# Kernel tuning notes

Hardware: AMD Instinct MI355X
Metric: run time of the kernel (lower is better)

The kernel has to match this reference:

```python
import jax, jax.numpy as jnp
import numpy as np

D = 256          # feature_dim
H = 4            # num_heads (hard-coded in AdaAttentionalPropagation)
HD = D // H      # per-head dim = 64
L = 6            # number of layers
B, N, M = 2, 2048, 2048
NAMES = ("self", "cross", "self", "cross", "self", "cross")
POOLS = (1, 1, 2, 2, 2, 2)
EPS = 1e-5


def conv1x1(W, b, x):
    # Conv1d kernel_size=1 == pointwise linear over channels: x [B, Cin, N] -> [B, Cout, N]
    return jnp.einsum('oi,bin->bon', W, x) + b[None, :, None]


def inst_norm(x):
    # InstanceNorm1d(affine=False): normalize over spatial dim per (batch, channel)
    mu = jnp.mean(x, axis=-1, keepdims=True)
    var = jnp.var(x, axis=-1, keepdims=True)
    return (x - mu) * jax.lax.rsqrt(var + EPS)


def attn_prop(params, x, source, mask):
    # One AdaAttentionalPropagation layer. x [B,D,Nq], source [B,D,Nk], mask [B,Nq,Nk]
    Wq, bq, Wk, bk, Wv, bv, Wm, bm, W1, b1, W2, b2 = params
    b = x.shape[0]
    q = conv1x1(Wq, bq, x).reshape(b, HD, H, -1)       # [B, hd, H, Nq]
    k = conv1x1(Wk, bk, source).reshape(b, HD, H, -1)  # [B, hd, H, Nk]
    v = conv1x1(Wv, bv, source).reshape(b, HD, H, -1)
    scores = jnp.einsum('bdhn,bdhm->bhnm', q, k) / np.sqrt(HD).astype(np.float32)
    scores = scores * mask[:, None]                     # multiplicative pruned mask
    prob = jax.nn.softmax(scores, axis=-1)              # [B, H, Nq, Nk]
    att = jnp.einsum('bhnm,bdhm->bdhn', prob, v).reshape(b, D, -1)
    message = conv1x1(Wm, bm, att)                      # merge
    y = jnp.concatenate([x, message], axis=1)           # [B, 2D, Nq]
    h = jax.nn.relu(inst_norm(conv1x1(W1, b1, y)))      # MLP_IN hidden
    delta = conv1x1(W2, b2, h)                          # [B, D, Nq]
    return delta, jnp.mean(prob, axis=1)                # prob averaged over heads


def prune(conn, prob, pool, k_cur):
    # update_connections_by_pooling_size: keep top (k_cur // pool) entries per row
    if prob is None or pool == 1:
        return conn, k_cur
    k_new = k_cur // pool
    vals, idxs = jax.lax.top_k(prob, k_new)             # over last axis
    b, n, _ = conn.shape
    new = jnp.zeros_like(conn).at[
        jnp.arange(b)[:, None, None], jnp.arange(n)[None, :, None], idxs
    ].set(jnp.where(vals > 0, 1.0, 0.0).astype(conn.dtype))
    return jax.lax.stop_gradient(new), k_new


def setup_inputs() -> dict:
    key = jax.random.key(0)
    ks = jax.random.split(key, 16)
    s1 = 1.0 / np.sqrt(D)
    s2 = 1.0 / np.sqrt(2 * D)
    return {
        "desc0": jax.random.normal(ks[0], (B, D, N), dtype=jnp.float32),
        "desc1": jax.random.normal(ks[1], (B, D, M), dtype=jnp.float32),
        "Wq": jax.random.normal(ks[2], (L, D, D), dtype=jnp.float32) * s1,
        "bq": jax.random.normal(ks[3], (L, D), dtype=jnp.float32) * 0.01,
        "Wk": jax.random.normal(ks[4], (L, D, D), dtype=jnp.float32) * s1,
        "bk": jax.random.normal(ks[5], (L, D), dtype=jnp.float32) * 0.01,
        "Wv": jax.random.normal(ks[6], (L, D, D), dtype=jnp.float32) * s1,
        "bv": jax.random.normal(ks[7], (L, D), dtype=jnp.float32) * 0.01,
        "Wm": jax.random.normal(ks[8], (L, D, D), dtype=jnp.float32) * s1,
        "bm": jax.random.normal(ks[9], (L, D), dtype=jnp.float32) * 0.01,
        "W1": jax.random.normal(ks[10], (L, 2 * D, 2 * D), dtype=jnp.float32) * s2,
        "b1": jax.random.normal(ks[11], (L, 2 * D), dtype=jnp.float32) * 0.01,
        "W2": jax.random.normal(ks[12], (L, D, 2 * D), dtype=jnp.float32) * s2,
        "b2": jnp.zeros((L, D), dtype=jnp.float32),  # nn.init.constant_(mlp[-1].bias, 0)
    }


def reference(desc0, desc1, Wq, bq, Wk, bk, Wv, bv, Wm, bm, W1, b1, W2, b2):
    b = desc0.shape[0]
    n, m = desc0.shape[2], desc1.shape[2]
    masks = {
        '00': jnp.ones((b, n, n), jnp.float32), '01': jnp.ones((b, n, m), jnp.float32),
        '11': jnp.ones((b, m, m), jnp.float32), '10': jnp.ones((b, m, n), jnp.float32),
    }
    probs = {'00': None, '01': None, '11': None, '10': None}
    kcnt = {'00': n, '01': m, '11': m, '10': n}
    for i in range(L):
        params = (Wq[i], bq[i], Wk[i], bk[i], Wv[i], bv[i],
                  Wm[i], bm[i], W1[i], b1[i], W2[i], b2[i])
        pool = POOLS[i]
        if NAMES[i] == 'cross':
            masks['01'], kcnt['01'] = prune(masks['01'], probs['01'], pool, kcnt['01'])
            delta0, probs['01'] = attn_prop(params, desc0, desc1, masks['01'])
            masks['10'], kcnt['10'] = prune(masks['10'], probs['10'], pool, kcnt['10'])
            delta1, probs['10'] = attn_prop(params, desc1, desc0, masks['10'])
        else:
            masks['00'], kcnt['00'] = prune(masks['00'], probs['00'], pool, kcnt['00'])
            delta0, probs['00'] = attn_prop(params, desc0, desc0, masks['00'])
            masks['11'], kcnt['11'] = prune(masks['11'], probs['11'], pool, kcnt['11'])
            delta1, probs['11'] = attn_prop(params, desc1, desc1, masks['11'])
        desc0 = desc0 + delta0
        desc1 = desc1 + delta1
    return jnp.stack([desc0, desc1])  # [2, B, D, N]
```

## Files before the change

kernel.cpp:

```cpp
#include <hip/hip_runtime.h>
#include <hip/hip_bf16.h>
#include <stdint.h>

#define NPTS 2048
#define MB_ROW 256L
#define MB_B   ((long)NPTS * MB_ROW)
#define MB_T   (2 * MB_B)

typedef __attribute__((ext_vector_type(8))) short bf16x8;
typedef __attribute__((ext_vector_type(4))) float f32x4;
#define MFMA16 __builtin_amdgcn_mfma_f32_16x16x32_bf16

__device__ inline unsigned short f2b(float f) {
  union { float f; unsigned int u; } x; x.f = f;
  unsigned int u = x.u;
  return (unsigned short)((u + 0x7FFFu + ((u >> 16) & 1u)) >> 16);
}
__device__ inline float bfu(unsigned int us) {
  union { unsigned int u; float f; } x; x.u = (us & 0xFFFFu) << 16;
  return x.f;
}
__device__ inline void sp3(float x, unsigned short& h, unsigned short& m, unsigned short& l) {
  h = f2b(x);
  float r1 = x - bfu(h);
  m = f2b(r1);
  l = f2b(r1 - bfu(m));
}
__device__ inline void gld16(const unsigned short* g, unsigned short* l) {
  __builtin_amdgcn_global_load_lds(
      (const __attribute__((address_space(1))) void*)g,
      (__attribute__((address_space(3))) void*)l, 16, 0, 0);
}
__device__ inline int swzF(int F) { return F ^ ((F >> 3) & 7); }

#define E_P3  0
#define E_V3  1
#define E_S3  2
#define E_Y3  3
#define E_H   4
#define E_RES 5
#define E_S3S 6

template <int EPI>
__global__ __launch_bounds__(256) void t3_k(
    const unsigned short* __restrict__ A, long aps,
    const unsigned short* __restrict__ B, long bps,
    const unsigned short* __restrict__ B2, long b2ps,
    const float* __restrict__ bias,
    void* __restrict__ out,
    const unsigned char* __restrict__ masks,
    int K, int lda, int ldb, int ksplit, long sps,
    int zbase, int xorv, int selfl, int yoff) {
  const int t = threadIdx.x;
  const int z = blockIdx.z;
  const int zg = zbase + z;
  long aoff = 0, boff = 0, b2off = 0;
  if constexpr (EPI == E_P3 || EPI == E_V3) {
    boff = (long)z * 524288;
  } else if constexpr (EPI == E_S3 || EPI == E_S3S) {
    const int sb = zg >> 2, h = zg & 3;
    aoff = (long)zg * 131072;
    boff = (long)((sb ^ xorv) * 4 + h) * 131072;
  } else if constexpr (EPI == E_Y3) {
    boff = (long)zg * 524288;
  } else if constexpr (EPI == E_H) {
    boff = (long)zg * 524288;
    b2off = (long)z * 524288;
  } else {
    boff = (long)z * 1048576;
  }
  const int n0 = blockIdx.x * 64;
  const int m0 = ((EPI == E_S3 || EPI == E_S3S) ? yoff : 0) + blockIdx.y * 64;

  __shared__ __align__(16) unsigned short As[3][64 * 64];
  __shared__ __align__(16) unsigned short Bs[3][64 * 64];
  __shared__ unsigned int Ms[128];
  if constexpr (EPI == E_S3 || EPI == E_S3S) {
    if (t < 128) {
      const int sb = zg >> 2;
      const int type = selfl ? (sb >> 1) : 2 + (sb >> 1);
      const unsigned int* mw =
          (const unsigned int*)(masks + (long)type * MB_T + (long)(sb & 1) * MB_B);
      Ms[t] = mw[(long)(m0 + (t >> 1)) * 64 + (n0 >> 5) + (t & 1)];
    }
  }

  const int w = t >> 6;
  const int L = t & 63;
  const int wm = (w & 1) * 32, wn = (w >> 1) * 32;
  const int lr = t & 15, lk = (t >> 4) & 3;
  const int swr = (lr & 7) << 3;
  const int grow = (L >> 3);
  const int gj = L & 7;

  f32x4 acc[2][2];
#pragma unroll
  for (int i = 0; i < 2; ++i)
#pragma unroll
    for (int j = 0; j < 2; ++j) acc[i][j] = (f32x4){0.f, 0.f, 0.f, 0.f};

  for (int k0 = 0; k0 < K; k0 += 64) {
    const unsigned short* Bsel;
    long bo, bp;
    int kb;
    if (k0 < ksplit) { Bsel = B; bo = boff; bp = bps; kb = k0; }
    else             { Bsel = B2; bo = b2off; bp = b2ps; kb = k0 - ksplit; }
    if (k0) __syncthreads();
#pragma unroll
    for (int pl = 0; pl < 3; ++pl) {
      const unsigned short* Ap = A + (long)pl * aps + aoff;
      const unsigned short* Bp = Bsel + (long)pl * bp + bo;
#pragma unroll
      for (int c = 0; c < 2; ++c) {
        const int rbase = w * 16 + c * 8;
        const int row = rbase + grow;
        const int colA = (gj ^ (row & 7)) << 3;
        gld16(&Ap[(long)(m0 + row) * lda + k0 + colA], &As[pl][rbase * 64]);
        gld16(&Bp[(long)(n0 + row) * ldb + kb + colA], &Bs[pl][rbase * 64]);
      }
    }
    __syncthreads();
#pragma unroll
    for (int kk = 0; kk < 2; ++kk) {
      bf16x8 af[3][2], bf[3][2];
#pragma unroll
      for (int pl = 0; pl < 3; ++pl)
#pragma unroll
        for (int mi = 0; mi < 2; ++mi) {
          af[pl][mi] = *(const bf16x8*)&As[pl][(wm + mi * 16 + lr) * 64 + ((kk * 32 + lk * 8) ^ swr)];
          bf[pl][mi] = *(const bf16x8*)&Bs[pl][(wn + mi * 16 + lr) * 64 + ((kk * 32 + lk * 8) ^ swr)];
        }
#pragma unroll
      for (int mi = 0; mi < 2; ++mi)
#pragma unroll
        for (int ni = 0; ni < 2; ++ni) {
          f32x4 c = acc[mi][ni];
          c = MFMA16(af[2][mi], bf[0][ni], c, 0, 0, 0);
          c = MFMA16(af[0][mi], bf[2][ni], c, 0, 0, 0);
          c = MFMA16(af[1][mi], bf[1][ni], c, 0, 0, 0);
          c = MFMA16(af[1][mi], bf[0][ni], c, 0, 0, 0);
          c = MFMA16(af[0][mi], bf[1][ni], c, 0, 0, 0);
          c = MFMA16(af[0][mi], bf[0][ni], c, 0, 0, 0);
          acc[mi][ni] = c;
        }
    }
  }

  if constexpr (EPI == E_S3 || EPI == E_S3S) {
    __syncthreads();
    float* ST = (float*)&As[0][0];
#pragma unroll
    for (int mi = 0; mi < 2; ++mi)
#pragma unroll
      for (int ni = 0; ni < 2; ++ni)
#pragma unroll
        for (int r = 0; r < 4; ++r)
          ST[(wm + mi * 16 + lk * 4 + r) * 68 + wn + ni * 16 + lr] = acc[mi][ni][r];
    __syncthreads();
    float* o = (float*)out;
#pragma unroll
    for (int it = 0; it < 4; ++it) {
      const int row = (t >> 4) + it * 16;
      const int col = (t & 15) * 4;
      float4 vv = *(const float4*)&ST[row * 68 + col];
      const unsigned int mw = Ms[row * 2 + (col >> 5)];
      vv.x = ((mw >> ((col + 0) & 31)) & 1u) ? vv.x * 0.125f : 0.f;
      vv.y = ((mw >> ((col + 1) & 31)) & 1u) ? vv.y * 0.125f : 0.f;
      vv.z = ((mw >> ((col + 2) & 31)) & 1u) ? vv.z * 0.125f : 0.f;
      vv.w = ((mw >> ((col + 3) & 31)) & 1u) ? vv.w * 0.125f : 0.f;
      const int rloc = blockIdx.y * 64 + row;
      *(float4*)&o[(long)z * sps + (long)rloc * 2048 + n0 + col] = vv;
      if constexpr (EPI == E_S3S) {
        float2* pst = (float2*)const_cast<float*>(bias);
        const int CHrows = (int)(sps >> 11);
        float mx4 = fmaxf(fmaxf(vv.x, vv.y), fmaxf(vv.z, vv.w));
#pragma unroll
        for (int oo = 1; oo < 16; oo <<= 1) mx4 = fmaxf(mx4, __shfl_xor(mx4, oo));
        float e4 = __expf(vv.x - mx4) + __expf(vv.y - mx4) +
                   __expf(vv.z - mx4) + __expf(vv.w - mx4);
#pragma unroll
        for (int oo = 1; oo < 16; oo <<= 1) e4 += __shfl_xor(e4, oo);
        if ((t & 15) == 0)
          pst[((long)z * CHrows + rloc) * 32 + blockIdx.x] = make_float2(mx4, e4);
      }
    }
    return;
  }

#pragma unroll
  for (int mi = 0; mi < 2; ++mi) {
#pragma unroll
    for (int ni = 0; ni < 2; ++ni) {
      f32x4 a = acc[mi][ni];
      const int cM = m0 + wm + mi * 16 + lk * 4;
      const int pN = n0 + wn + ni * 16 + lr;
      if constexpr (EPI == E_P3) {
        float4 bv4 = *(const float4*)&bias[cM];
        float bb[4] = {bv4.x, bv4.y, bv4.z, bv4.w};
        unsigned short* o = (unsigned short*)out;
        const long b0 = (long)z * 524288 + (long)pN * 64 + (cM >> 2);
#pragma unroll
        for (int r = 0; r < 4; ++r) {
          unsigned short h_, m_, l_;
          sp3(a[r] + bb[r], h_, m_, l_);
          const long ad = b0 + (long)r * 131072;
          o[ad] = h_; o[ad + 2097152] = m_; o[ad + 4194304] = l_;
        }
      } else if constexpr (EPI == E_V3) {
        float4 bv4 = *(const float4*)&bias[cM];
        float bb[4] = {bv4.x, bv4.y, bv4.z, bv4.w};
        unsigned short* o = (unsigned short*)out;
        const long b0 = (long)z * 524288 + (long)(cM >> 2) * 2048 + pN;
#pragma unroll
        for (int r = 0; r < 4; ++r) {
          unsigned short h_, m_, l_;
          sp3(a[r] + bb[r], h_, m_, l_);
          const long ad = b0 + (long)r * 131072;
          o[ad] = h_; o[ad + 2097152] = m_; o[ad + 4194304] = l_;
        }
      } else if constexpr (EPI == E_Y3) {
        float4 bv4 = *(const float4*)&bias[cM];
        float bb[4] = {bv4.x, bv4.y, bv4.z, bv4.w};
        unsigned short* o = (unsigned short*)out;
        ushort4 h4, m4, l4;
        unsigned short* hp = (unsigned short*)&h4;
        unsigned short* mp = (unsigned short*)&m4;
        unsigned short* lp = (unsigned short*)&l4;
#pragma unroll
        for (int r = 0; r < 4; ++r) sp3(a[r] + bb[r], hp[r], mp[r], lp[r]);
        const long b0 = (long)z * 524288 + (long)pN * 256 + cM;
        *(ushort4*)&o[b0] = h4;
        *(ushort4*)&o[b0 + sps] = m4;
        *(ushort4*)&o[b0 + 2 * sps] = l4;
      } else if constexpr (EPI == E_H) {
        *(f32x4*)&((float*)out)[(long)z * 1048576 + (long)pN * 512 + cM] = a;
      } else {
        float4 bv4 = *(const float4*)&bias[cM];
        float* p = &((float*)out)[(long)zg * 524288 + (long)pN * 256 + cM];
        float4 old = *(const float4*)p;
        float4 nw;
        nw.x = old.x + a[0] + bv4.x; nw.y = old.y + a[1] + bv4.y;
        nw.z = old.z + a[2] + bv4.z; nw.w = old.w + a[3] + bv4.w;
        *(float4*)p = nw;
      }
    }
  }
}

__global__ __launch_bounds__(256) void stat_k(const float2* __restrict__ pst,
                                              float2* __restrict__ stats) {
  const int idx = blockIdx.x * 256 + threadIdx.x;
  const float2* p = pst + (long)idx * 32;
  float m = p[0].x;
#pragma unroll
  for (int i = 1; i < 32; ++i) m = fmaxf(m, p[i].x);
  float s = 0.f;
#pragma unroll
  for (int i = 0; i < 32; ++i) s += p[i].y * __expf(p[i].x - m);
  stats[idx] = make_float2(m, 1.0f / s);
}

__global__ __launch_bounds__(256) void softmax_prune_k(
    const float* __restrict__ S, float2* __restrict__ stats,
    unsigned char* __restrict__ masks,
    int knew, int sbG, int cb, int selfl, long sps, int CH) {
  const int t = threadIdx.x;
  const int lane = t & 63;
  const int wv = t >> 6;
  const int nl = blockIdx.x;

  __shared__ __align__(16) float4 pL4[4][512];
  __shared__ int hist[256];
  __shared__ int wred[4];
  __shared__ int sbx[2];

  {
    const float* row = S + (long)wv * sps + (long)nl * 2048 + lane * 32;
    float xs[32];
#pragma unroll
    for (int e = 0; e < 8; ++e) {
      float4 u = *(const float4*)(row + e * 4);
      xs[e * 4 + 0] = u.x; xs[e * 4 + 1] = u.y;
      xs[e * 4 + 2] = u.z; xs[e * 4 + 3] = u.w;
    }
    float m = xs[0];
#pragma unroll
    for (int j = 1; j < 32; ++j) m = fmaxf(m, xs[j]);
    for (int o = 32; o; o >>= 1) m = fmaxf(m, __shfl_xor(m, o));
    float s = 0.f;
#pragma unroll
    for (int j = 0; j < 32; ++j) { xs[j] = __expf(xs[j] - m); s += xs[j]; }
    for (int o = 32; o; o >>= 1) s += __shfl_xor(s, o);
    const float ri = 1.0f / s;
    if (lane == 0) stats[(long)wv * CH + nl] = make_float2(m, ri);
#pragma unroll
    for (int e = 0; e < 8; ++e) {
      float4 pv;
      pv.x = xs[e * 4 + 0] * ri; pv.y = xs[e * 4 + 1] * ri;
      pv.z = xs[e * 4 + 2] * ri; pv.w = xs[e * 4 + 3] * ri;
      pL4[wv][swzF(lane * 8 + e)] = pv;
    }
  }
  __syncthreads();

  unsigned int key[8];
  {
#pragma unroll
    for (int jj = 0; jj < 2; ++jj) {
      const int Fs = swzF(t * 2 + jj);
      float4 p0 = pL4[0][Fs];
      float4 p1 = pL4[1][Fs];
      float4 p2 = pL4[2][Fs];
      float4 p3 = pL4[3][Fs];
      float4 mm;
      mm.x = 0.25f * p0.x; mm.x += 0.25f * p1.x; mm.x += 0.25f * p2.x; mm.x += 0.25f * p3.x;
      mm.y = 0.25f * p0.y; mm.y += 0.25f * p1.y; mm.y += 0.25f * p2.y; mm.y += 0.25f * p3.y;
      mm.z = 0.25f * p0.z; mm.z += 0.25f * p1.z; mm.z += 0.25f * p2.z; mm.z += 0.25f * p3.z;
      mm.w = 0.25f * p0.w; mm.w += 0.25f * p1.w; mm.w += 0.25f * p2.w; mm.w += 0.25f * p3.w;
      key[jj * 4 + 0] = __float_as_uint(mm.x);
      key[jj * 4 + 1] = __float_as_uint(mm.y);
      key[jj * 4 + 2] = __float_as_uint(mm.z);
      key[jj * 4 + 3] = __float_as_uint(mm.w);
    }
  }

  unsigned int pref = 0;
  int kneed = knew;
  for (int pass = 0; pass < 4; ++pass) {
    const int shift = 24 - pass * 8;
    hist[t] = 0;
    __syncthreads();
    const unsigned int hm = (pass == 0) ? 0u : (0xFFFFFFFFu << (shift + 8));
#pragma unroll
    for (int j = 0; j < 8; ++j) {
      unsigned int k = key[j];
      if ((k & hm) == pref) atomicAdd(&hist[(k >> shift) & 255], 1);
    }
    __syncthreads();
    const int h = hist[t];
    int s = h;
#pragma unroll
    for (int o = 1; o < 64; o <<= 1) {
      int tmp = __shfl_down(s, o);
      if (lane + o < 64) s += tmp;
    }
    if (lane == 0) wred[wv] = s;
    __syncthreads();
    int addhi = 0;
#pragma unroll
    for (int w2 = 0; w2 < 4; ++w2)
      if (w2 > wv) addhi += wred[w2];
    s += addhi;
    const int above = s - h;
    if (s >= kneed && above < kneed) { sbx[0] = t; sbx[1] = above; }
    __syncthreads();
    pref |= ((unsigned int)sbx[0]) << shift;
    kneed -= sbx[1];
    __syncthreads();
  }
  const unsigned int T = pref;
  const int take = kneed;
  int cnt = 0;
#pragma unroll
  for (int j = 0; j < 8; ++j) cnt += (key[j] == T);
  int pc = cnt;
#pragma unroll
  for (int o = 1; o < 64; o <<= 1) {
    int tmp = __shfl_up(pc, o);
    if (lane >= o) pc += tmp;
  }
  if (lane == 63) wred[wv] = pc;
  __syncthreads();
  int woff = 0;
#pragma unroll
  for (int w2 = 0; w2 < 4; ++w2)
    if (w2 < wv) woff += wred[w2];
  int base = woff + pc - cnt;
  unsigned int byte = 0;
#pragma unroll
  for (int j = 0; j < 8; ++j) {
    unsigned int k = key[j];
    int sel = 0;
    if (k > T) sel = 1;
    else if (k == T) { if (T > 0u && base < take) sel = 1; base++; }
    byte |= (unsigned int)sel << j;
  }
  const int type = selfl ? (sbG >> 1) : 2 + (sbG >> 1);
  unsigned char* mb = masks + (long)type * MB_T + (long)(sbG & 1) * MB_B;
  mb[(long)(cb + nl) * MB_ROW + t] = (unsigned char)byte;
}

__global__ __launch_bounds__(256) void pv3_k(
    const unsigned short* __restrict__ V3, const float* __restrict__ S, long sps,
    const float2* __restrict__ stats, int CH,
    float* __restrict__ part, int zbase, int xorv) {
  const int t = threadIdx.x;
  const int h = blockIdx.z;
  const int kseg = blockIdx.y;
  const int n0 = blockIdx.x * 64;
  const int sb = zbase >> 2;
  const unsigned short* Vb = V3 + (long)((sb ^ xorv) * 4 + h) * 131072;
  const float* Sp = S + (long)h * sps;
  const float2* sth = stats + (long)h * CH;

  __shared__ __align__(16) unsigned short Bs[3][64 * 64];

  const int w = t >> 6;
  const int wm = (w & 1) * 32, wn = (w >> 1) * 32;
  const int lr = t & 15, lk = (t >> 4) & 3;
  const int srow = t >> 3, scol = (t & 7) * 8;
  const int sws = scol ^ ((srow & 7) << 3);
  const int swr = (lr & 7) << 3;

  f32x4 acc[2][2];
#pragma unroll
  for (int i = 0; i < 2; ++i)
#pragma unroll
    for (int j = 0; j < 2; ++j) acc[i][j] = (f32x4){0.f, 0.f, 0.f, 0.f};

  const int kbeg = kseg * 256;
  const float2 st0 = sth[n0 + srow];
  const float2 st1 = sth[n0 + 32 + srow];
  const float* srcA = &Sp[(long)(n0 + srow) * 2048 + kbeg + scol];
  const float* srcB = &Sp[(long)(n0 + 32 + srow) * 2048 + kbeg + scol];

  float4 c0a = *(const float4*)srcA;
  float4 c0b = *(const float4*)(srcA + 4);
  float4 c1a = *(const float4*)srcB;
  float4 c1b = *(const float4*)(srcB + 4);

#pragma unroll
  for (int ki = 0; ki < 4; ++ki) {
    const int k0 = kbeg + ki * 64;
    float4 n0a, n0b, n1a, n1b;
    if (ki < 3) {
      const int off = (ki + 1) * 64;
      n0a = *(const float4*)(srcA + off);
      n0b = *(const float4*)(srcA + off + 4);
      n1a = *(const float4*)(srcB + off);
      n1b = *(const float4*)(srcB + off + 4);
    }
    if (ki) __syncthreads();
    {
      float xs[8] = {c0a.x, c0a.y, c0a.z, c0a.w, c0b.x, c0b.y, c0b.z, c0b.w};
      ushort4 hq[2], mq[2], lq[2];
      unsigned short* hp = (unsigned short*)hq;
      unsigned short* mp = (unsigned short*)mq;
      unsigned short* lp = (unsigned short*)lq;
#pragma unroll
      for (int j = 0; j < 8; ++j) {
        float p = __expf(xs[j] - st0.x) * st0.y;
        sp3(p, hp[j], mp[j], lp[j]);
      }
      *(ushort4*)&Bs[0][srow * 64 + sws] = hq[0];
      *(ushort4*)&Bs[0][srow * 64 + sws + 4] = hq[1];
      *(ushort4*)&Bs[1][srow * 64 + sws] = mq[0];
      *(ushort4*)&Bs[1][srow * 64 + sws + 4] = mq[1];
      *(ushort4*)&Bs[2][srow * 64 + sws] = lq[0];
      *(ushort4*)&Bs[2][srow * 64 + sws + 4] = lq[1];
    }
    {
      float xs[8] = {c1a.x, c1a.y, c1a.z, c1a.w, c1b.x, c1b.y, c1b.z, c1b.w};
      ushort4 hq[2], mq[2], lq[2];
      unsigned short* hp = (unsigned short*)hq;
      unsigned short* mp = (unsigned short*)mq;
      unsigned short* lp = (unsigned short*)lq;
#pragma unroll
      for (int j = 0; j < 8; ++j) {
        float p = __expf(xs[j] - st1.x) * st1.y;
        sp3(p, hp[j], mp[j], lp[j]);
      }
      const int rr = 32 + srow;
      *(ushort4*)&Bs[0][rr * 64 + sws] = hq[0];
      *(ushort4*)&Bs[0][rr * 64 + sws + 4] = hq[1];
      *(ushort4*)&Bs[1][rr * 64 + sws] = mq[0];
      *(ushort4*)&Bs[1][rr * 64 + sws + 4] = mq[1];
      *(ushort4*)&Bs[2][rr * 64 + sws] = lq[0];
      *(ushort4*)&Bs[2][rr * 64 + sws + 4] = lq[1];
    }
    __syncthreads();
#pragma unroll
    for (int kk = 0; kk < 2; ++kk) {
      bf16x8 af[3][2], bf[3][2];
#pragma unroll
      for (int pl = 0; pl < 3; ++pl) {
#pragma unroll
        for (int mi = 0; mi < 2; ++mi) {
          af[pl][mi] = *(const bf16x8*)&Vb[(long)pl * 2097152 +
                                           (long)(wm + mi * 16 + lr) * 2048 + k0 + kk * 32 + lk * 8];
          bf[pl][mi] = *(const bf16x8*)&Bs[pl][(wn + mi * 16 + lr) * 64 + ((kk * 32 + lk * 8) ^ swr)];
        }
      }
#pragma unroll
      for (int mi = 0; mi < 2; ++mi)
#pragma unroll
        for (int ni = 0; ni < 2; ++ni) {
          f32x4 c = acc[mi][ni];
          c = MFMA16(af[2][mi], bf[0][ni], c, 0, 0, 0);
          c = MFMA16(af[0][mi], bf[2][ni], c, 0, 0, 0);
          c = MFMA16(af[1][mi], bf[1][ni], c, 0, 0, 0);
          c = MFMA16(af[1][mi], bf[0][ni], c, 0, 0, 0);
          c = MFMA16(af[0][mi], bf[1][ni], c, 0, 0, 0);
          c = MFMA16(af[0][mi], bf[0][ni], c, 0, 0, 0);
          acc[mi][ni] = c;
        }
    }
    if (ki < 3) { c0a = n0a; c0b = n0b; c1a = n1a; c1b = n1b; }
  }

  float* pp = part + (((long)kseg * 4 + h) * CH) * 64;
#pragma unroll
  for (int mi = 0; mi < 2; ++mi) {
#pragma unroll
    for (int ni = 0; ni < 2; ++ni) {
      const int cM = wm + mi * 16 + lk * 4;
      const int pN = n0 + wn + ni * 16 + lr;
      *(f32x4*)&pp[(long)pN * 64 + cM] = acc[mi][ni];
    }
  }
}

__global__ __launch_bounds__(256) void comb_k(const float* __restrict__ part,
                                              unsigned short* __restrict__ att3,
                                              int CH, int sb, int cb) {
  const int q = threadIdx.x & 63;
  const int g = threadIdx.x >> 6;
  const int nl = blockIdx.x * 4 + g;
  float s[4] = {0.f, 0.f, 0.f, 0.f};
#pragma unroll
  for (int ks = 0; ks < 8; ++ks)
#pragma unroll
    for (int h = 0; h < 4; ++h)
      s[h] += part[(((long)ks * 4 + h) * CH + nl) * 64 + q];
  ushort4 h4, m4, l4;
  unsigned short* hp = (unsigned short*)&h4;
  unsigned short* mp = (unsigned short*)&m4;
  unsigned short* lp = (unsigned short*)&l4;
#pragma unroll
  for (int h = 0; h < 4; ++h) sp3(s[h], hp[h], mp[h], lp[h]);
  const long base = (long)sb * 524288 + (long)(cb + nl) * 256 + 4 * q;
  *(ushort4*)&att3[base] = h4;
  *(ushort4*)&att3[base + 2097152] = m4;
  *(ushort4*)&att3[base + 4194304] = l4;
}

__global__ __launch_bounds__(256) void inormA_k(const float* __restrict__ H,
                                                float* __restrict__ partial) {
  const int seg = blockIdx.x, sbl = blockIdx.y;
  const float* hp = H + (long)sbl * 1048576;
  const int t = threadIdx.x;
  float s0 = 0.f, q0 = 0.f, s1 = 0.f, q1 = 0.f;
  const int r0 = seg * 64;
  for (int r = r0; r < r0 + 64; ++r) {
    float x0 = hp[(long)r * 512 + t];
    float x1 = hp[(long)r * 512 + t + 256];
    s0 += x0; q0 = fmaf(x0, x0, q0);
    s1 += x1; q1 = fmaf(x1, x1, q1);
  }
  float* pp = partial + ((long)sbl * 32 + seg) * 1024;
  pp[t] = s0; pp[t + 256] = s1;
  pp[512 + t] = q0; pp[512 + t + 256] = q1;
}

__global__ __launch_bounds__(256) void inormB_k(const float* __restrict__ partial,
                                                float* __restrict__ stats2) {
  const int sbl = blockIdx.x;
  const int t = threadIdx.x;
  const float* pp = partial + (long)sbl * 32768;
  float a0 = 0.f, b0 = 0.f, a1 = 0.f, b1 = 0.f;
  for (int seg = 0; seg < 32; ++seg) {
    const float* p = pp + seg * 1024;
    a0 += p[t]; a1 += p[t + 256];
    b0 += p[512 + t]; b1 += p[512 + t + 256];
  }
  float mu0 = a0 * (1.f / 2048.f);
  float mu1 = a1 * (1.f / 2048.f);
  float rs0 = rsqrtf(b0 * (1.f / 2048.f) - mu0 * mu0 + 1e-5f);
  float rs1 = rsqrtf(b1 * (1.f / 2048.f) - mu1 * mu1 + 1e-5f);
  float* st = stats2 + (long)sbl * 1024;
  st[t] = mu0; st[t + 256] = mu1;
  st[512 + t] = rs0; st[512 + t + 256] = rs1;
}

__global__ __launch_bounds__(256) void inormC_k(const float* __restrict__ H,
                                                const float* __restrict__ stats2,
                                                unsigned short* __restrict__ HB,
                                                long hps) {
  const int seg = blockIdx.x, sbl = blockIdx.y;
  const float* hp = H + (long)sbl * 1048576;
  unsigned short* hb = HB + (long)sbl * 1048576;
  const float* st = stats2 + (long)sbl * 1024;
  const int t = threadIdx.x;
  const float mu0 = st[t], mu1 = st[t + 256];
  const float rs0 = st[512 + t], rs1 = st[512 + t + 256];
  const int r0 = seg * 64;
  for (int r = r0; r < r0 + 64; ++r) {
    float x0 = hp[(long)r * 512 + t];
    float x1 = hp[(long)r * 512 + t + 256];
    float o0 = (x0 - mu0) * rs0; o0 = o0 > 0.f ? o0 : 0.f;
    float o1 = (x1 - mu1) * rs1; o1 = o1 > 0.f ? o1 : 0.f;
    unsigned short h_, m_, l_;
    sp3(o0, h_, m_, l_);
    const long ad0 = (long)r * 512 + t;
    hb[ad0] = h_; hb[ad0 + hps] = m_; hb[ad0 + 2 * hps] = l_;
    sp3(o1, h_, m_, l_);
    const long ad1 = ad0 + 256;
    hb[ad1] = h_; hb[ad1 + hps] = m_; hb[ad1 + 2 * hps] = l_;
  }
}

__global__ __launch_bounds__(256) void split6_k(
    const float* __restrict__ q, const float* __restrict__ k,
    const float* __restrict__ v, const float* __restrict__ m,
    const float* __restrict__ w1, const float* __restrict__ w2,
    unsigned short* __restrict__ dst) {
  long i = ((long)blockIdx.x * 256 + threadIdx.x) * 4;
  const float* src;
  long off, base, ps;
  if (i < 262144) {
    int sel = (int)(i >> 16);
    src = sel == 0 ? q : sel == 1 ? k : sel == 2 ? v : m;
    off = i & 65535; base = (long)sel * 196608; ps = 65536;
  } else if (i < 524288) {
    src = w1; off = i - 262144; base = 786432; ps = 262144;
  } else {
    src = w2; off = i - 524288; base = 1572864; ps = 131072;
  }
  float4 vv = *(const float4*)&src[off];
  float xs[4] = {vv.x, vv.y, vv.z, vv.w};
  ushort4 h4, m4, l4;
  unsigned short* hp = (unsigned short*)&h4;
  unsigned short* mp = (unsigned short*)&m4;
  unsigned short* lp = (unsigned short*)&l4;
#pragma unroll
  for (int j = 0; j < 4; ++j) sp3(xs[j], hp[j], mp[j], lp[j]);
  *(ushort4*)&dst[base + off] = h4;
  *(ushort4*)&dst[base + ps + off] = m4;
  *(ushort4*)&dst[base + 2 * ps + off] = l4;
}

__global__ __launch_bounds__(256) void split3_k(const float* __restrict__ src,
                                                unsigned short* __restrict__ dst,
                                                long plane, long n) {
  long i = ((long)blockIdx.x * 256 + threadIdx.x) * 4;
  if (i >= n) return;
  float4 v = *(const float4*)&src[i];
  float xs[4] = {v.x, v.y, v.z, v.w};
  ushort4 h4, m4, l4;
  unsigned short* hp = (unsigned short*)&h4;
  unsigned short* mp = (unsigned short*)&m4;
  unsigned short* lp = (unsigned short*)&l4;
#pragma unroll
  for (int j = 0; j < 4; ++j) sp3(xs[j], hp[j], mp[j], lp[j]);
  *(ushort4*)&dst[i] = h4;
  *(ushort4*)&dst[plane + i] = m4;
  *(ushort4*)&dst[2 * plane + i] = l4;
}

__global__ __launch_bounds__(256) void tin_k(const float* __restrict__ d0,
                                             const float* __restrict__ d1,
                                             float* __restrict__ descT) {
  __shared__ float tl[32][33];
  const int sb = blockIdx.z, s = sb >> 1, b = sb & 1;
  const float* src = (s ? d1 : d0) + (long)b * 524288;
  const int p0 = blockIdx.x * 32, c0 = blockIdx.y * 32;
  const int tx = threadIdx.x & 31, ty = threadIdx.x >> 5;
#pragma unroll
  for (int i = 0; i < 4; ++i)
    tl[ty + i * 8][tx] = src[(long)(c0 + ty + i * 8) * 2048 + p0 + tx];
  __syncthreads();
#pragma unroll
  for (int i = 0; i < 4; ++i)
    descT[(long)sb * 524288 + (long)(p0 + ty + i * 8) * 256 + c0 + tx] = tl[tx][ty + i * 8];
}

__global__ __launch_bounds__(256) void tout_k(const float* __restrict__ descT,
                                              float* __restrict__ out) {
  __shared__ float tl[32][33];
  const int sb = blockIdx.z;
  const int p0 = blockIdx.x * 32, c0 = blockIdx.y * 32;
  const int tx = threadIdx.x & 31, ty = threadIdx.x >> 5;
#pragma unroll
  for (int i = 0; i < 4; ++i)
    tl[ty + i * 8][tx] = descT[(long)sb * 524288 + (long)(p0 + ty + i * 8) * 256 + c0 + tx];
  __syncthreads();
#pragma unroll
  for (int i = 0; i < 4; ++i)
    out[(long)sb * 524288 + (long)(c0 + ty + i * 8) * 2048 + p0 + tx] = tl[tx][ty + i * 8];
}

extern "C" void kernel_launch(void* const* d_in, const int* in_sizes, int n_in,
                              void* d_out, int out_size, void* d_ws, size_t ws_size,
                              hipStream_t stream) {
  (void)in_sizes; (void)n_in; (void)out_size;
  const float* in_d0 = (const float*)d_in[0];
  const float* in_d1 = (const float*)d_in[1];
  const float* Wq = (const float*)d_in[2];
  const float* bq = (const float*)d_in[3];
  const float* Wk = (const float*)d_in[4];
  const float* bk = (const float*)d_in[5];
  const float* Wv = (const float*)d_in[6];
  const float* bv = (const float*)d_in[7];
  const float* Wm = (const float*)d_in[8];
  const float* bm = (const float*)d_in[9];
  const float* W1 = (const float*)d_in[10];
  const float* b1 = (const float*)d_in[11];
  const float* W2 = (const float*)d_in[12];
  const float* b2 = (const float*)d_in[13];
  (void)b1;

  const long region_b = (long)ws_size - 79429632;
  const int CH = (region_b >= 40992L * 2048) ? 2048
               : (region_b >= 40992L * 1024) ? 1024 : 512;
  const int nchunks = 2048 / CH;
  const long sps = (long)CH * 2048;
  const int mb = (region_b >= 4 * 13766656L) ? 4 : (region_b >= 2 * 13766656L) ? 2 : 1;

  uint8_t* w = (uint8_t*)d_ws;
  float* descT          = (float*)w;
  unsigned short* desc3 = (unsigned short*)(w + 8388608);
  unsigned short* Q3    = (unsigned short*)(w + 20971520);
  unsigned short* K3    = (unsigned short*)(w + 33554432);
  unsigned short* V3    = (unsigned short*)(w + 46137344);
  unsigned short* att3  = (unsigned short*)(w + 58720256);
  unsigned short* wbuf  = (unsigned short*)(w + 71303168);
  unsigned char* masks  = w + 75235328;
  uint8_t* region       = w + 79429632;
  float* S              = (float*)region;
  float* part           = (float*)(region + (long)CH * 32768);
  float2* pst           = (float2*)part;
  float2* stats         = (float2*)(region + (long)CH * 32768 + (long)CH * 8192);
  unsigned short* msg3  = (unsigned short*)region;
  float* hbuf           = (float*)(region + (long)mb * 3145728);
  unsigned short* hB3   = (unsigned short*)(region + (long)mb * 7340032);
  float* inpart         = (float*)(region + (long)mb * 13631488);
  float* instats        = (float*)(region + (long)mb * 13631488 + (long)mb * 131072);

  const unsigned short* wq3 = wbuf;
  const unsigned short* wk3 = wbuf + 196608;
  const unsigned short* wv3 = wbuf + 393216;
  const unsigned short* wm3 = wbuf + 589824;
  const unsigned short* w13 = wbuf + 786432;
  const unsigned short* w23 = wbuf + 1572864;

  tin_k<<<dim3(64, 8, 4), 256, 0, stream>>>(in_d0, in_d1, descT);
  hipMemsetAsync(masks, 0xFF, 4 * MB_T, stream);

  for (int l = 0; l < 6; ++l) {
    const int selfl = (l % 2 == 0);
    const int xorv = selfl ? 0 : 2;
    const int knew = (l < 2) ? 1024 : (l < 4) ? 512 : 0;

    split6_k<<<dim3(640), 256, 0, stream>>>(Wq + (long)l * 65536, Wk + (long)l * 65536,
                                            Wv + (long)l * 65536, Wm + (long)l * 65536,
                                            W1 + (long)l * 262144, W2 + (long)l * 131072,
                                            wbuf);
    split3_k<<<dim3(2048), 256, 0, stream>>>(descT, desc3, 2097152, 2097152);

    t3_k<E_P3><<<dim3(32, 4, 4), 256, 0, stream>>>(
        wq3, 65536, desc3, 2097152, nullptr, 0, bq + l * 256, Q3, nullptr,
        256, 256, 256, 1 << 30, 0, 0, 0, 0, 0);
    t3_k<E_P3><<<dim3(32, 4, 4), 256, 0, stream>>>(
        wk3, 65536, desc3, 2097152, nullptr, 0, bk + l * 256, K3, nullptr,
        256, 256, 256, 1 << 30, 0, 0, 0, 0, 0);
    t3_k<E_V3><<<dim3(32, 4, 4), 256, 0, stream>>>(
        wv3, 65536, desc3, 2097152, nullptr, 0, bv + l * 256, V3, nullptr,
        256, 256, 256, 1 << 30, 0, 0, 0, 0, 0);

    for (int sb = 0; sb < 4; ++sb) {
      for (int c = 0; c < nchunks; ++c) {
        const int cb = c * CH;
        if (knew) {
          t3_k<E_S3><<<dim3(32, CH / 64, 4), 256, 0, stream>>>(
              Q3, 2097152, K3, 2097152, nullptr, 0, nullptr, S, masks,
              64, 64, 64, 1 << 30, sps, sb * 4, xorv, selfl, cb);
          softmax_prune_k<<<dim3(CH), 256, 0, stream>>>(
              S, stats, masks, knew, sb, cb, selfl, sps, CH);
        } else {
          t3_k<E_S3S><<<dim3(32, CH / 64, 4), 256, 0, stream>>>(
              Q3, 2097152, K3, 2097152, nullptr, 0, (const float*)pst, S, masks,
              64, 64, 64, 1 << 30, sps, sb * 4, xorv, selfl, cb);
          stat_k<<<dim3(4 * CH / 256), 256, 0, stream>>>(pst, stats);
        }
        pv3_k<<<dim3(CH / 64, 8, 4), 256, 0, stream>>>(V3, S, sps, stats, CH, part, sb * 4, xorv);
        comb_k<<<dim3(CH / 4), 256, 0, stream>>>(part, att3, CH, sb, cb);
      }
    }

    for (int p = 0; p < 4; p += mb) {
      t3_k<E_Y3><<<dim3(32, 4, mb), 256, 0, stream>>>(
          wm3, 65536, att3, 2097152, nullptr, 0, bm + l * 256, msg3, nullptr,
          256, 256, 256, 1 << 30, (long)mb * 524288, p, 0, 0, 0);
      t3_k<E_H><<<dim3(32, 8, mb), 256, 0, stream>>>(
          w13, 262144, desc3, 2097152, msg3, (long)mb * 524288, nullptr, hbuf, nullptr,
          512, 512, 256, 256, 0, p, 0, 0, 0);
      inormA_k<<<dim3(32, mb), 256, 0, stream>>>(hbuf, inpart);
      inormB_k<<<dim3(mb), 256, 0, stream>>>(inpart, instats);
      inormC_k<<<dim3(32, mb), 256, 0, stream>>>(hbuf, instats, hB3, (long)mb * 1048576);
      t3_k<E_RES><<<dim3(32, 4, mb), 256, 0, stream>>>(
          w23, 131072, hB3, (long)mb * 1048576, nullptr, 0, b2 + l * 256, descT, nullptr,
          512, 512, 512, 1 << 30, 0, p, 0, 0, 0);
    }
  }

  tout_k<<<dim3(64, 8, 4), 256, 0, stream>>>(descT, (float*)d_out);
}
```

Before: 2.834 ms.

## Split QK^T score GEMM into dedicated kernel with 64x128 tiles

Moves the attention score (QK^T) GEMM out of the generic t3_k template into a dedicated s3w_k kernel. Each block now computes a 64x128 tile instead of 64x64, and the whole K=64 slab of all three bf16 split planes is loaded into LDS once, with no k-loop. The wider tile lets each Q fragment be reused across four N sub-tiles and halves the grid. In exchange it uses more LDS and registers per block, which may lower occupancy. The mask, scale and partial-softmax-stats epilogue is widened to 8 columns per thread, writing two stat entries per 128-wide tile so the stat_k layout stays the same.

```diff
diff --git a/kernel.cpp b/kernel.cpp
--- a/kernel.cpp
+++ b/kernel.cpp
@@ -35,11 +35,9 @@
 
 #define E_P3  0
 #define E_V3  1
-#define E_S3  2
 #define E_Y3  3
 #define E_H   4
 #define E_RES 5
-#define E_S3S 6
 
 template <int EPI>
 __global__ __launch_bounds__(256) void t3_k(
@@ -57,10 +55,6 @@
   long aoff = 0, boff = 0, b2off = 0;
   if constexpr (EPI == E_P3 || EPI == E_V3) {
     boff = (long)z * 524288;
-  } else if constexpr (EPI == E_S3 || EPI == E_S3S) {
-    const int sb = zg >> 2, h = zg & 3;
-    aoff = (long)zg * 131072;
-    boff = (long)((sb ^ xorv) * 4 + h) * 131072;
   } else if constexpr (EPI == E_Y3) {
     boff = (long)zg * 524288;
   } else if constexpr (EPI == E_H) {
@@ -70,20 +64,10 @@
     boff = (long)z * 1048576;
   }
   const int n0 = blockIdx.x * 64;
-  const int m0 = ((EPI == E_S3 || EPI == E_S3S) ? yoff : 0) + blockIdx.y * 64;
+  const int m0 = blockIdx.y * 64;
 
   __shared__ __align__(16) unsigned short As[3][64 * 64];
   __shared__ __align__(16) unsigned short Bs[3][64 * 64];
-  __shared__ unsigned int Ms[128];
-  if constexpr (EPI == E_S3 || EPI == E_S3S) {
-    if (t < 128) {
-      const int sb = zg >> 2;
-      const int type = selfl ? (sb >> 1) : 2 + (sb >> 1);
-      const unsigned int* mw =
-          (const unsigned int*)(masks + (long)type * MB_T + (long)(sb & 1) * MB_B);
-      Ms[t] = mw[(long)(m0 + (t >> 1)) * 64 + (n0 >> 5) + (t & 1)];
-    }
-  }
 
   const int w = t >> 6;
   const int L = t & 63;
@@ -144,47 +128,6 @@
           acc[mi][ni] = c;
         }
     }
-  }
-
-  if constexpr (EPI == E_S3 || EPI == E_S3S) {
-    __syncthreads();
-    float* ST = (float*)&As[0][0];
-#pragma unroll
-    for (int mi = 0; mi < 2; ++mi)
-#pragma unroll
-      for (int ni = 0; ni < 2; ++ni)
-#pragma unroll
-        for (int r = 0; r < 4; ++r)
-          ST[(wm + mi * 16 + lk * 4 + r) * 68 + wn + ni * 16 + lr] = acc[mi][ni][r];
-    __syncthreads();
-    float* o = (float*)out;
-#pragma unroll
-    for (int it = 0; it < 4; ++it) {
-      const int row = (t >> 4) + it * 16;
-      const int col = (t & 15) * 4;
-      float4 vv = *(const float4*)&ST[row * 68 + col];
-      const unsigned int mw = Ms[row * 2 + (col >> 5)];
-      vv.x = ((mw >> ((col + 0) & 31)) & 1u) ? vv.x * 0.125f : 0.f;
-      vv.y = ((mw >> ((col + 1) & 31)) & 1u) ? vv.y * 0.125f : 0.f;
-      vv.z = ((mw >> ((col + 2) & 31)) & 1u) ? vv.z * 0.125f : 0.f;
-      vv.w = ((mw >> ((col + 3) & 31)) & 1u) ? vv.w * 0.125f : 0.f;
-      const int rloc = blockIdx.y * 64 + row;
-      *(float4*)&o[(long)z * sps + (long)rloc * 2048 + n0 + col] = vv;
-      if constexpr (EPI == E_S3S) {
-        float2* pst = (float2*)const_cast<float*>(bias);
-        const int CHrows = (int)(sps >> 11);
-        float mx4 = fmaxf(fmaxf(vv.x, vv.y), fmaxf(vv.z, vv.w));
-#pragma unroll
-        for (int oo = 1; oo < 16; oo <<= 1) mx4 = fmaxf(mx4, __shfl_xor(mx4, oo));
-        float e4 = __expf(vv.x - mx4) + __expf(vv.y - mx4) +
-                   __expf(vv.z - mx4) + __expf(vv.w - mx4);
-#pragma unroll
-        for (int oo = 1; oo < 16; oo <<= 1) e4 += __shfl_xor(e4, oo);
-        if ((t & 15) == 0)
-          pst[((long)z * CHrows + rloc) * 32 + blockIdx.x] = make_float2(mx4, e4);
-      }
-    }
-    return;
   }
 
 #pragma unroll
@@ -243,6 +186,145 @@
         nw.z = old.z + a[2] + bv4.z; nw.w = old.w + a[3] + bv4.w;
         *(float4*)p = nw;
       }
+    }
+  }
+}
+
+template <int STATS>
+__global__ __launch_bounds__(256) void s3w_k(
+    const unsigned short* __restrict__ Q3, const unsigned short* __restrict__ K3,
+    float* __restrict__ S, float2* __restrict__ pst,
+    const unsigned char* __restrict__ masks,
+    long sps, int zbase, int xorv, int selfl, int yoff) {
+  const int t = threadIdx.x;
+  const int z = blockIdx.z;
+  const int zg = zbase + z;
+  const int sb = zg >> 2, h = zg & 3;
+  const long aoff = (long)zg * 131072;
+  const long boff = (long)((sb ^ xorv) * 4 + h) * 131072;
+  const int n0 = blockIdx.x * 128;
+  const int m0 = yoff + blockIdx.y * 64;
+
+  __shared__ __align__(16) unsigned short sh[3 * 4096 + 3 * 8192];
+  unsigned short* Asp = sh;
+  unsigned short* Bsp = sh + 12288;
+  __shared__ unsigned int Ms[256];
+  {
+    const int type = selfl ? (sb >> 1) : 2 + (sb >> 1);
+    const unsigned int* mw =
+        (const unsigned int*)(masks + (long)type * MB_T + (long)(sb & 1) * MB_B);
+    Ms[t] = mw[(long)(m0 + (t >> 2)) * 64 + (n0 >> 5) + (t & 3)];
+  }
+
+  const int w = t >> 6;
+  const int L = t & 63;
+  const int lr = t & 15, lk = (t >> 4) & 3;
+  const int swr = (lr & 7) << 3;
+  const int grow = L >> 3;
+  const int gj = L & 7;
+  const int wm = (w & 1) * 32, wn = (w >> 1) * 64;
+
+#pragma unroll
+  for (int pl = 0; pl < 3; ++pl) {
+    const unsigned short* Ap = Q3 + (long)pl * 2097152 + aoff;
+    const unsigned short* Bp = K3 + (long)pl * 2097152 + boff;
+#pragma unroll
+    for (int c = 0; c < 2; ++c) {
+      const int rbase = w * 16 + c * 8;
+      const int row = rbase + grow;
+      const int colA = (gj ^ (row & 7)) << 3;
+      gld16(&Ap[(long)(m0 + row) * 64 + colA], &Asp[pl * 4096 + rbase * 64]);
+    }
+#pragma unroll
+    for (int c = 0; c < 4; ++c) {
+      const int rbase = w * 32 + c * 8;
+      const int row = rbase + grow;
+      const int colA = (gj ^ (row & 7)) << 3;
+      gld16(&Bp[(long)(n0 + row) * 64 + colA], &Bsp[pl * 8192 + rbase * 64]);
+    }
+  }
+  __syncthreads();
+
+  f32x4 acc[2][4];
+#pragma unroll
+  for (int i = 0; i < 2; ++i)
+#pragma unroll
+    for (int j = 0; j < 4; ++j) acc[i][j] = (f32x4){0.f, 0.f, 0.f, 0.f};
+
+#pragma unroll
+  for (int kk = 0; kk < 2; ++kk) {
+    bf16x8 af[3][2];
+#pragma unroll
+    for (int pl = 0; pl < 3; ++pl)
+#pragma unroll
+      for (int mi = 0; mi < 2; ++mi)
+        af[pl][mi] = *(const bf16x8*)&Asp[pl * 4096 + (wm + mi * 16 + lr) * 64 + ((kk * 32 + lk * 8) ^ swr)];
+#pragma unroll
+    for (int ni = 0; ni < 4; ++ni) {
+      bf16x8 bfx[3];
+#pragma unroll
+      for (int pl = 0; pl < 3; ++pl)
+        bfx[pl] = *(const bf16x8*)&Bsp[pl * 8192 + (wn + ni * 16 + lr) * 64 + ((kk * 32 + lk * 8) ^ swr)];
+#pragma unroll
+      for (int mi = 0; mi < 2; ++mi) {
+        f32x4 c = acc[mi][ni];
+        c = MFMA16(af[2][mi], bfx[0], c, 0, 0, 0);
+        c = MFMA16(af[0][mi], bfx[2], c, 0, 0, 0);
+        c = MFMA16(af[1][mi], bfx[1], c, 0, 0, 0);
+        c = MFMA16(af[1][mi], bfx[0], c, 0, 0, 0);
+        c = MFMA16(af[0][mi], bfx[1], c, 0, 0, 0);
+        c = MFMA16(af[0][mi], bfx[0], c, 0, 0, 0);
+        acc[mi][ni] = c;
+      }
+    }
+  }
+
+  __syncthreads();
+  float* ST = (float*)sh;
+#pragma unroll
+  for (int mi = 0; mi < 2; ++mi)
+#pragma unroll
+    for (int ni = 0; ni < 4; ++ni)
+#pragma unroll
+      for (int r = 0; r < 4; ++r)
+        ST[(wm + mi * 16 + lk * 4 + r) * 132 + wn + ni * 16 + lr] = acc[mi][ni][r];
+  __syncthreads();
+  float* o = S;
+  const int CHrows = (int)(sps >> 11);
+#pragma unroll
+  for (int it = 0; it < 4; ++it) {
+    const int row = (t >> 4) + it * 16;
+    const int col = (t & 15) * 8;
+    float4 v0 = *(const float4*)&ST[row * 132 + col];
+    float4 v1 = *(const float4*)&ST[row * 132 + col + 4];
+    const unsigned int mw = Ms[row * 4 + (col >> 5)];
+    v0.x = ((mw >> ((col + 0) & 31)) & 1u) ? v0.x * 0.125f : 0.f;
+    v0.y = ((mw >> ((col + 1) & 31)) & 1u) ? v0.y * 0.125f : 0.f;
+    v0.z = ((mw >> ((col + 2) & 31)) & 1u) ? v0.z * 0.125f : 0.f;
+    v0.w = ((mw >> ((col + 3) & 31)) & 1u) ? v0.w * 0.125f : 0.f;
+    v1.x = ((mw >> ((col + 4) & 31)) & 1u) ? v1.x * 0.125f : 0.f;
+    v1.y = ((mw >> ((col + 5) & 31)) & 1u) ? v1.y * 0.125f : 0.f;
+    v1.z = ((mw >> ((col + 6) & 31)) & 1u) ? v1.z * 0.125f : 0.f;
+    v1.w = ((mw >> ((col + 7) & 31)) & 1u) ? v1.w * 0.125f : 0.f;
+    const int rloc = blockIdx.y * 64 + row;
+    *(float4*)&o[(long)z * sps + (long)rloc * 2048 + n0 + col] = v0;
+    *(float4*)&o[(long)z * sps + (long)rloc * 2048 + n0 + col + 4] = v1;
+    if constexpr (STATS) {
+      float mx8 = fmaxf(fmaxf(fmaxf(v0.x, v0.y), fmaxf(v0.z, v0.w)),
+                        fmaxf(fmaxf(v1.x, v1.y), fmaxf(v1.z, v1.w)));
+      mx8 = fmaxf(mx8, __shfl_xor(mx8, 1));
+      mx8 = fmaxf(mx8, __shfl_xor(mx8, 2));
+      mx8 = fmaxf(mx8, __shfl_xor(mx8, 4));
+      float e8 = __expf(v0.x - mx8) + __expf(v0.y - mx8) +
+                 __expf(v0.z - mx8) + __expf(v0.w - mx8) +
+                 __expf(v1.x - mx8) + __expf(v1.y - mx8) +
+                 __expf(v1.z - mx8) + __expf(v1.w - mx8);
+      e8 += __shfl_xor(e8, 1);
+      e8 += __shfl_xor(e8, 2);
+      e8 += __shfl_xor(e8, 4);
+      if ((t & 7) == 0)
+        pst[((long)z * CHrows + rloc) * 32 + blockIdx.x * 2 + ((t >> 3) & 1)] =
+            make_float2(mx8, e8);
     }
   }
 }
@@ -771,15 +853,13 @@
       for (int c = 0; c < nchunks; ++c) {
         const int cb = c * CH;
         if (knew) {
-          t3_k<E_S3><<<dim3(32, CH / 64, 4), 256, 0, stream>>>(
-              Q3, 2097152, K3, 2097152, nullptr, 0, nullptr, S, masks,
-              64, 64, 64, 1 << 30, sps, sb * 4, xorv, selfl, cb);
+          s3w_k<0><<<dim3(16, CH / 64, 4), 256, 0, stream>>>(
+              Q3, K3, S, pst, masks, sps, sb * 4, xorv, selfl, cb);
           softmax_prune_k<<<dim3(CH), 256, 0, stream>>>(
               S, stats, masks, knew, sb, cb, selfl, sps, CH);
         } else {
-          t3_k<E_S3S><<<dim3(32, CH / 64, 4), 256, 0, stream>>>(
-              Q3, 2097152, K3, 2097152, nullptr, 0, (const float*)pst, S, masks,
-              64, 64, 64, 1 << 30, sps, sb * 4, xorv, selfl, cb);
+          s3w_k<1><<<dim3(16, CH / 64, 4), 256, 0, stream>>>(
+              Q3, K3, S, pst, masks, sps, sb * 4, xorv, selfl, cb);
           stat_k<<<dim3(4 * CH / 256), 256, 0, stream>>>(pst, stats);
         }
         pv3_k<<<dim3(CH / 64, 8, 4), 256, 0, stream>>>(V3, S, sps, stats, CH, part, sb * 4, xorv);
```

Measured after the change: 2.906 ms. 2.6% more time.
